# Optimization experiments

Hardware: AMD Instinct MI355X
Metric: run time of the kernel (lower is better)

Reference implementation:

```python
import jax, jax.numpy as jnp
import numpy as np

RADIUS = 8
EPS = 0.005

_DN = ('NCHW', 'OIHW', 'NCHW')

def _box_filter(t, r):
    """Separable normalized box filter with reflect padding. t: [H, W]."""
    ks = 2 * r + 1
    tp = jnp.pad(t, ((r, r), (r, r)), mode='reflect')[None, None]  # [1,1,H+2r,W+2r]
    kh = jnp.ones((1, 1, 1, ks), t.dtype) / ks
    kv = jnp.ones((1, 1, ks, 1), t.dtype) / ks
    out = jax.lax.conv_general_dilated(tp, kh, (1, 1), 'VALID', dimension_numbers=_DN)
    out = jax.lax.conv_general_dilated(out, kv, (1, 1), 'VALID', dimension_numbers=_DN)
    return out[0, 0]  # [H, W]

def setup_inputs() -> dict:
    key = jax.random.key(0)
    x = jax.random.uniform(key, (4096, 4096, 3), dtype=jnp.float32)
    return {"x": x}

def reference(x):
    # Rec.709 luma
    Y = 0.2126 * x[..., 0] + 0.7152 * x[..., 1] + 0.0722 * x[..., 2]  # [H,W]
    mean_I = _box_filter(Y, RADIUS)
    mean_II = _box_filter(Y * Y, RADIUS)
    var_I = mean_II - mean_I * mean_I
    a = var_I / (var_I + EPS)
    b = mean_I - a * mean_I
    mean_a = _box_filter(a, RADIUS)
    mean_b = _box_filter(b, RADIUS)
    Y_smooth = mean_a * Y + mean_b
    scale = (Y_smooth / jnp.maximum(Y, 1e-6))[..., None]  # [H,W,1]
    return jnp.clip(x * scale, 0.0, 1.0)
```

## Files before the change

### kernel.cpp

```cpp
#include <hip/hip_runtime.h>
#include <hip/hip_fp16.h>


#define HH 4096
#define WW 4096
#define TW 32
#define TH 64
#define SW 64
#define SH 96
#define SYS 65
#define HIS 49
#define HAS 33
#define INV289 (1.0f / 289.0f)
#define EPSV 0.005f

__device__ __forceinline__ int reflect_idx(int i, int n) {
    i = (i < 0) ? -i : i;
    i = (i >= n) ? (2 * n - 2 - i) : i;
    return i;
}

__global__ __launch_bounds__(256) void gf_fused(const float* __restrict__ x,
                                                float* __restrict__ out) {
    __shared__ float sY[SH * SYS];
    __shared__ float hI[SH * HIS];
    __shared__ float hII[SH * HIS];
    const int t = threadIdx.x;
    const int tx = blockIdx.x * TW;
    const int ty = blockIdx.y * TH;

    const bool interior = (tx >= 16) & (tx + 48 <= WW) & (ty >= 16) & (ty + 80 <= HH);
    if (interior) {
        for (int idx = t; idx < SH * SW; idx += 256) {
            int r = idx >> 6, c = idx & 63;
            const float* p = x + (((ty + r - 16) * WW) + (tx + c - 16)) * 3;
            sY[r * SYS + c] = 0.2126f * p[0] + 0.7152f * p[1] + 0.0722f * p[2];
        }
    } else {
        for (int idx = t; idx < SH * SW; idx += 256) {
            int r = idx >> 6, c = idx & 63;
            int gy = reflect_idx(ty + r - 16, HH);
            int gx = reflect_idx(tx + c - 16, WW);
            const float* p = x + (gy * WW + gx) * 3;
            sY[r * SYS + c] = 0.2126f * p[0] + 0.7152f * p[1] + 0.0722f * p[2];
        }
    }
    __syncthreads();

    for (int task = t; task < SH * 3; task += 256) {
        int r = task % SH;
        int s = task / SH;
        int base = r * SYS + s * 16;
        int ob = r * HIS + s * 16;
        float sI = 0.f, sII = 0.f;
        #pragma unroll
        for (int k = 0; k <= 16; ++k) { float w = sY[base + k]; sI += w; sII += w * w; }
        hI[ob] = sI; hII[ob] = sII;
        #pragma unroll
        for (int j = 1; j < 16; ++j) {
            float va = sY[base + 16 + j];
            float vs = sY[base + j - 1];
            sI  += va - vs;
            sII += va * va - vs * vs;
            hI[ob + j] = sI; hII[ob + j] = sII;
        }
    }
    __syncthreads();

    __half2* ab = (__half2*)sY;
    if (t < 240) {
        int c = t % 48;
        int q = t / 48;
        int r0 = q * 16;
        float sI = 0.f, sII = 0.f;
        #pragma unroll
        for (int k = 0; k <= 16; ++k) {
            sI  += hI[(r0 + k) * HIS + c];
            sII += hII[(r0 + k) * HIS + c];
        }
        #pragma unroll
        for (int j = 0; j < 16; ++j) {
            int o = r0 + j;
            float mI = sI * INV289;
            float mII = sII * INV289;
            float var = mII - mI * mI;
            float a = var / (var + EPSV);
            float b = mI - a * mI;
            ab[o * HIS + c] = __floats2half2_rn(a, b);
            if (j < 15) {
                sI  += hI[(o + 17) * HIS + c] - hI[o * HIS + c];
                sII += hII[(o + 17) * HIS + c] - hII[o * HIS + c];
            }
        }
    }
    __syncthreads();

    float* hA = hI;
    float* hB = hII;
    if (t < 160) {
        int r = t % 80;
        int s = t / 80;
        int base = r * HIS + s * 16;
        int ob = r * HAS + s * 16;
        float sA = 0.f, sB = 0.f;
        #pragma unroll
        for (int k = 0; k <= 16; ++k) {
            float2 v = __half22float2(ab[base + k]);
            sA += v.x; sB += v.y;
        }
        hA[ob] = sA; hB[ob] = sB;
        #pragma unroll
        for (int j = 1; j < 16; ++j) {
            float2 va = __half22float2(ab[base + 16 + j]);
            float2 vs = __half22float2(ab[base + j - 1]);
            sA += va.x - vs.x;
            sB += va.y - vs.y;
            hA[ob + j] = sA; hB[ob + j] = sB;
        }
    }
    __syncthreads();

    {
        int c = t & 31;
        int q = t >> 5;
        int r0 = q * 8;
        float sA = 0.f, sB = 0.f;
        #pragma unroll
        for (int k = 0; k <= 16; ++k) {
            sA += hA[(r0 + k) * HAS + c];
            sB += hB[(r0 + k) * HAS + c];
        }
        #pragma unroll
        for (int j = 0; j < 8; ++j) {
            int o = r0 + j;
            float ma = sA * INV289;
            float mb = sB * INV289;
            int gy = ty + o, gx = tx + c;
            const float* p = x + (gy * WW + gx) * 3;
            float rr = p[0], gg = p[1], bb = p[2];
            float Y = 0.2126f * rr + 0.7152f * gg + 0.0722f * bb;
            float scale = (ma * Y + mb) / fmaxf(Y, 1e-6f);
            float* qo = out + (gy * WW + gx) * 3;
            qo[0] = fminf(fmaxf(rr * scale, 0.f), 1.f);
            qo[1] = fminf(fmaxf(gg * scale, 0.f), 1.f);
            qo[2] = fminf(fmaxf(bb * scale, 0.f), 1.f);
            if (j < 7) {
                sA += hA[(o + 17) * HAS + c] - hA[o * HAS + c];
                sB += hB[(o + 17) * HAS + c] - hB[o * HAS + c];
            }
        }
    }
}

extern "C" void kernel_launch(void* const* d_in, const int* in_sizes, int n_in,
                              void* d_out, int out_size, void* d_ws, size_t ws_size,
                              hipStream_t stream) {
    const float* x = (const float*)d_in[0];
    float* out = (float*)d_out;
    dim3 grid(WW / TW, HH / TH);
    gf_fused<<<grid, 256, 0, stream>>>(x, out);
}
```

Measured before the change: 400.7 us.

## Store all shared-memory intermediates as fp16 to raise occupancy

```diff
diff --git a/kernel.cpp b/kernel.cpp
--- a/kernel.cpp
+++ b/kernel.cpp
@@ -20,29 +20,36 @@
     return i;
 }
 
-__global__ __launch_bounds__(256) void gf_fused(const float* __restrict__ x,
-                                                float* __restrict__ out) {
-    __shared__ float sY[SH * SYS];
-    __shared__ float hI[SH * HIS];
-    __shared__ float hII[SH * HIS];
+__global__ __launch_bounds__(256, 4) void gf_fused(const float* __restrict__ x,
+                                                   float* __restrict__ out) {
+    __shared__ __align__(16) char smem[15680 + 18816];
+    __half*  sY    = (__half*)smem;
+    __half2* ab    = (__half2*)smem;
+    __half2* hIhII = (__half2*)(smem + 15680);
+    __half2* hAhB  = (__half2*)(smem + 15680);
+
     const int t = threadIdx.x;
     const int tx = blockIdx.x * TW;
     const int ty = blockIdx.y * TH;
 
-    const bool interior = (tx >= 16) & (tx + 48 <= WW) & (ty >= 16) & (ty + 80 <= HH);
-    if (interior) {
-        for (int idx = t; idx < SH * SW; idx += 256) {
-            int r = idx >> 6, c = idx & 63;
-            const float* p = x + (((ty + r - 16) * WW) + (tx + c - 16)) * 3;
-            sY[r * SYS + c] = 0.2126f * p[0] + 0.7152f * p[1] + 0.0722f * p[2];
-        }
-    } else {
-        for (int idx = t; idx < SH * SW; idx += 256) {
-            int r = idx >> 6, c = idx & 63;
-            int gy = reflect_idx(ty + r - 16, HH);
-            int gx = reflect_idx(tx + c - 16, WW);
-            const float* p = x + (gy * WW + gx) * 3;
-            sY[r * SYS + c] = 0.2126f * p[0] + 0.7152f * p[1] + 0.0722f * p[2];
+    {
+        const int c  = t & 63;
+        const int r0 = t >> 6;
+        const bool interior = (tx >= 16) & (tx + 48 <= WW) & (ty >= 16) & (ty + 80 <= HH);
+        if (interior) {
+            const float* p = x + ((long)(ty + r0 - 16) * WW + (tx + c - 16)) * 3;
+            for (int r = r0; r < SH; r += 4, p += 4 * WW * 3) {
+                float Yv = 0.2126f * p[0] + 0.7152f * p[1] + 0.0722f * p[2];
+                sY[r * SYS + c] = __float2half_rn(Yv);
+            }
+        } else {
+            const int gx = reflect_idx(tx + c - 16, WW);
+            for (int r = r0; r < SH; r += 4) {
+                int gy = reflect_idx(ty + r - 16, HH);
+                const float* p = x + ((long)gy * WW + gx) * 3;
+                float Yv = 0.2126f * p[0] + 0.7152f * p[1] + 0.0722f * p[2];
+                sY[r * SYS + c] = __float2half_rn(Yv);
+            }
         }
     }
     __syncthreads();
@@ -54,20 +61,22 @@
         int ob = r * HIS + s * 16;
         float sI = 0.f, sII = 0.f;
         #pragma unroll
-        for (int k = 0; k <= 16; ++k) { float w = sY[base + k]; sI += w; sII += w * w; }
-        hI[ob] = sI; hII[ob] = sII;
+        for (int k = 0; k <= 16; ++k) {
+            float w = __half2float(sY[base + k]);
+            sI += w; sII += w * w;
+        }
+        hIhII[ob] = __floats2half2_rn(sI, sII);
         #pragma unroll
         for (int j = 1; j < 16; ++j) {
-            float va = sY[base + 16 + j];
-            float vs = sY[base + j - 1];
+            float va = __half2float(sY[base + 16 + j]);
+            float vs = __half2float(sY[base + j - 1]);
             sI  += va - vs;
             sII += va * va - vs * vs;
-            hI[ob + j] = sI; hII[ob + j] = sII;
+            hIhII[ob + j] = __floats2half2_rn(sI, sII);
         }
     }
     __syncthreads();
 
-    __half2* ab = (__half2*)sY;
     if (t < 240) {
         int c = t % 48;
         int q = t / 48;
@@ -75,8 +84,8 @@
         float sI = 0.f, sII = 0.f;
         #pragma unroll
         for (int k = 0; k <= 16; ++k) {
-            sI  += hI[(r0 + k) * HIS + c];
-            sII += hII[(r0 + k) * HIS + c];
+            float2 v = __half22float2(hIhII[(r0 + k) * HIS + c]);
+            sI += v.x; sII += v.y;
         }
         #pragma unroll
         for (int j = 0; j < 16; ++j) {
@@ -88,15 +97,15 @@
             float b = mI - a * mI;
             ab[o * HIS + c] = __floats2half2_rn(a, b);
             if (j < 15) {
-                sI  += hI[(o + 17) * HIS + c] - hI[o * HIS + c];
-                sII += hII[(o + 17) * HIS + c] - hII[o * HIS + c];
+                float2 va = __half22float2(hIhII[(o + 17) * HIS + c]);
+                float2 vs = __half22float2(hIhII[o * HIS + c]);
+                sI  += va.x - vs.x;
+                sII += va.y - vs.y;
             }
         }
     }
     __syncthreads();
 
-    float* hA = hI;
-    float* hB = hII;
     if (t < 160) {
         int r = t % 80;
         int s = t / 80;
@@ -108,14 +117,14 @@
             float2 v = __half22float2(ab[base + k]);
             sA += v.x; sB += v.y;
         }
-        hA[ob] = sA; hB[ob] = sB;
+        hAhB[ob] = __floats2half2_rn(sA, sB);
         #pragma unroll
         for (int j = 1; j < 16; ++j) {
             float2 va = __half22float2(ab[base + 16 + j]);
             float2 vs = __half22float2(ab[base + j - 1]);
             sA += va.x - vs.x;
             sB += va.y - vs.y;
-            hA[ob + j] = sA; hB[ob + j] = sB;
+            hAhB[ob + j] = __floats2half2_rn(sA, sB);
         }
     }
     __syncthreads();
@@ -127,8 +136,8 @@
         float sA = 0.f, sB = 0.f;
         #pragma unroll
         for (int k = 0; k <= 16; ++k) {
-            sA += hA[(r0 + k) * HAS + c];
-            sB += hB[(r0 + k) * HAS + c];
+            float2 v = __half22float2(hAhB[(r0 + k) * HAS + c]);
+            sA += v.x; sB += v.y;
         }
         #pragma unroll
         for (int j = 0; j < 8; ++j) {
@@ -136,17 +145,19 @@
             float ma = sA * INV289;
             float mb = sB * INV289;
             int gy = ty + o, gx = tx + c;
-            const float* p = x + (gy * WW + gx) * 3;
+            const float* p = x + ((long)gy * WW + gx) * 3;
             float rr = p[0], gg = p[1], bb = p[2];
             float Y = 0.2126f * rr + 0.7152f * gg + 0.0722f * bb;
             float scale = (ma * Y + mb) / fmaxf(Y, 1e-6f);
-            float* qo = out + (gy * WW + gx) * 3;
+            float* qo = out + ((long)gy * WW + gx) * 3;
             qo[0] = fminf(fmaxf(rr * scale, 0.f), 1.f);
             qo[1] = fminf(fmaxf(gg * scale, 0.f), 1.f);
             qo[2] = fminf(fmaxf(bb * scale, 0.f), 1.f);
             if (j < 7) {
-                sA += hA[(o + 17) * HAS + c] - hA[o * HAS + c];
-                sB += hB[(o + 17) * HAS + c] - hB[o * HAS + c];
+                float2 va = __half22float2(hAhB[(o + 17) * HAS + c]);
+                float2 vs = __half22float2(hAhB[o * HAS + c]);
+                sA += va.x - vs.x;
+                sB += va.y - vs.y;
             }
         }
     }
```

Result: no change. 397.7 us (-0.8%).
